# Optimization experiments

Hardware: AMD Instinct MI355X
Metric: run time of the kernel (lower is better)

## Reference

```python
import jax, jax.numpy as jnp
import numpy as np

N_NODES = 1_000_000
FEAT = 128
CONTENT = 256
S2 = 8192          # seed layer (layer 2)
FAN = 8            # sampled neighbors per node (plus self)
S1 = S2 * (FAN + 1)    # 73728
S0 = S1 * (FAN + 1)    # 663552


def _block_edges(key, n_dst, n_src):
    # NodeFlow block: each dst node has a self-edge (its copy sits at the same
    # index in the source layer) plus FAN randomly sampled source neighbors.
    rand_src = jax.random.randint(key, (n_dst * FAN,), 0, n_src, dtype=jnp.int32)
    src = jnp.concatenate([jnp.arange(n_dst, dtype=jnp.int32), rand_src])
    dst = jnp.concatenate([jnp.arange(n_dst, dtype=jnp.int32),
                           jnp.repeat(jnp.arange(n_dst, dtype=jnp.int32), FAN)])
    return src, dst


def setup_inputs() -> dict:
    key = jax.random.key(0)
    ks = jax.random.split(key, 16)
    node_emb = jax.random.normal(ks[0], (N_NODES + 1, FEAT), jnp.float32) / FEAT
    content0 = jax.random.normal(ks[1], (S0, CONTENT), jnp.float32)
    Wp = jax.random.normal(ks[2], (FEAT, CONTENT), jnp.float32) * 0.05
    bp = jnp.zeros((FEAT,), jnp.float32)
    W0 = jax.random.normal(ks[3], (FEAT, 2 * FEAT), jnp.float32) * 0.05
    b0 = jnp.zeros((FEAT,), jnp.float32)
    Wagg0 = jax.random.normal(ks[4], (FEAT, FEAT), jnp.float32) * 0.05
    bagg0 = jnp.zeros((FEAT,), jnp.float32)
    W1 = jax.random.normal(ks[5], (FEAT, 2 * FEAT), jnp.float32) * 0.05
    b1 = jnp.zeros((FEAT,), jnp.float32)
    Wagg1 = jax.random.normal(ks[6], (FEAT, FEAT), jnp.float32) * 0.05
    bagg1 = jnp.zeros((FEAT,), jnp.float32)
    parent0 = jax.random.randint(ks[7], (S0,), 0, N_NODES, dtype=jnp.int32)
    src0, dst0 = _block_edges(ks[8], S1, S0)
    src1, dst1 = _block_edges(ks[9], S2, S1)
    return dict(node_emb=node_emb, content0=content0, Wp=Wp, bp=bp,
                W0=W0, b0=b0, Wagg0=Wagg0, bagg0=bagg0,
                W1=W1, b1=b1, Wagg1=Wagg1, bagg1=bagg1,
                parent0=parent0, src0=src0, dst0=dst0, src1=src1, dst1=dst1)


def _leaky(x):
    return jax.nn.leaky_relu(x, negative_slope=0.1)


def _conv(h_src, h_dst, src, dst, n_dst, W, b, Wagg, bagg, last):
    # message: copy_src('h'), copy_src('one'); reduce: sum -> h_agg, w
    agg = jax.ops.segment_sum(h_src[src], dst, num_segments=n_dst)
    w = jax.ops.segment_sum(jnp.ones((src.shape[0],), h_src.dtype), dst,
                            num_segments=n_dst)[:, None]
    h_agg = (agg - h_dst) / jnp.maximum(w - 1.0, 1.0)
    h_new = jnp.concatenate([h_dst, h_agg], axis=1) @ W.T + b
    h_a = h_agg @ Wagg.T + bagg
    if not last:
        h_new = _leaky(h_new)
        h_a = _leaky(h_a)
    h_new = h_new + h_a
    if last:  # prediction layer: no normalization
        return h_new
    norm = jnp.linalg.norm(h_new, axis=1, keepdims=True)
    return h_new / jnp.clip(norm, 1e-6)


def reference(node_emb, content0, Wp, bp, W0, b0, Wagg0, bagg0,
              W1, b1, Wagg1, bagg1, parent0, src0, dst0, src1, dst1):
    # init h per layer: node embedding + projected content (eval: no dropout/noise)
    h0 = node_emb[parent0 + 1] + _leaky(content0 @ Wp.T + bp)  # [S0, F]
    # layer 1 / 2 nodes are the first S1 / S2 entries of layer 0 (nested parents)
    h1_init = h0[:S1]
    h2_init = h0[:S2]
    h1 = _conv(h0, h1_init, src0, dst0, S1, W0, b0, Wagg0, bagg0, last=False)
    out = _conv(h1, h2_init, src1, dst1, S2, W1, b1, Wagg1, bagg1, last=True)
    return out
```

## Files before the change

kernel.cpp:

```cpp
#include <hip/hip_runtime.h>
#include <hip/hip_bf16.h>
#include <stdint.h>

#define S0N 663552
#define S1N 73728
#define S2N 8192

typedef __attribute__((ext_vector_type(8))) short bf16x8;
typedef __attribute__((ext_vector_type(4))) float floatx4;

static constexpr int LDK = 72;

__device__ __forceinline__ unsigned short f2b(float f) {
    union { float f; unsigned u; } v; v.f = f;
    unsigned r = v.u + 0x7fffu + ((v.u >> 16) & 1u);
    return (unsigned short)(r >> 16);
}
__device__ __forceinline__ float b2f(unsigned short h) {
    union { unsigned u; float f; } v; v.u = ((unsigned)h) << 16;
    return v.f;
}

__device__ __forceinline__ void stage_f32(const float* __restrict__ g, int rowStride,
                                          unsigned short* lds, int tid) {
    int r = tid >> 4;
    const int c = (tid & 15) << 2;
    #pragma unroll
    for (int it = 0; it < 8; ++it, r += 16) {
        const float4 v = *(const float4*)(g + (size_t)r * rowStride + c);
        unsigned short* d = &lds[r * LDK + c];
        d[0] = f2b(v.x); d[1] = f2b(v.y); d[2] = f2b(v.z); d[3] = f2b(v.w);
    }
}

__device__ __forceinline__ void stage_b16(const unsigned short* __restrict__ g, int rowStride,
                                          unsigned short* lds, int tid) {
    int r = tid >> 3;
    const int c = (tid & 7) << 3;
    #pragma unroll
    for (int it = 0; it < 4; ++it, r += 32) {
        const uint4 v = *(const uint4*)(g + (size_t)r * rowStride + c);
        *(uint4*)&lds[r * LDK + c] = v;
    }
}

__device__ __forceinline__ void mfma_128x128(const unsigned short* __restrict__ As,
                                             const unsigned short* __restrict__ Bs,
                                             floatx4 (&acc)[2][8],
                                             int wave, int l15, int quad) {
    #pragma unroll
    for (int kc = 0; kc < 64; kc += 32) {
        bf16x8 a[2], b[8];
        #pragma unroll
        for (int mt = 0; mt < 2; ++mt)
            a[mt] = *(const bf16x8*)&As[(wave * 32 + mt * 16 + l15) * LDK + kc + quad * 8];
        #pragma unroll
        for (int nt = 0; nt < 8; ++nt)
            b[nt] = *(const bf16x8*)&Bs[(nt * 16 + l15) * LDK + kc + quad * 8];
        #pragma unroll
        for (int mt = 0; mt < 2; ++mt)
            #pragma unroll
            for (int nt = 0; nt < 8; ++nt)
                acc[mt][nt] = __builtin_amdgcn_mfma_f32_16x16x32_bf16(a[mt], b[nt], acc[mt][nt], 0, 0, 0);
    }
}

__global__ __launch_bounds__(256, 2) void k_h0(
    const float* __restrict__ content, const float* __restrict__ Wp,
    const float* __restrict__ bp, const float* __restrict__ node_emb,
    const int* __restrict__ parent0, unsigned short* __restrict__ h0)
{
    __shared__ unsigned short As[128 * LDK];
    __shared__ unsigned short Bs[128 * LDK];
    const int tid = threadIdx.x;
    const int wave = tid >> 6, lane = tid & 63;
    const int l15 = lane & 15, quad = lane >> 4;
    const int row0 = blockIdx.x * 128;

    floatx4 acc[2][8];
    #pragma unroll
    for (int i = 0; i < 2; ++i)
        #pragma unroll
        for (int j = 0; j < 8; ++j) acc[i][j] = (floatx4)0.f;

    for (int k0 = 0; k0 < 256; k0 += 64) {
        stage_f32(content + (size_t)row0 * 256 + k0, 256, As, tid);
        stage_f32(Wp + k0, 256, Bs, tid);
        __syncthreads();
        mfma_128x128(As, Bs, acc, wave, l15, quad);
        __syncthreads();
    }

    #pragma unroll
    for (int mt = 0; mt < 2; ++mt) {
        #pragma unroll
        for (int r = 0; r < 4; ++r) {
            const int grow = row0 + wave * 32 + mt * 16 + quad * 4 + r;
            const int p = parent0[grow] + 1;
            const float* ne = node_emb + (size_t)p * 128;
            unsigned short* orow = h0 + (size_t)grow * 128;
            #pragma unroll
            for (int nt = 0; nt < 8; ++nt) {
                const int col = nt * 16 + l15;
                float v = acc[mt][nt][r] + bp[col];
                v = v > 0.f ? v : 0.1f * v;
                v += ne[col];
                orow[col] = f2b(v);
            }
        }
    }
}

__global__ __launch_bounds__(256, 4) void k_gather(
    const unsigned short* __restrict__ hsrc, const int* __restrict__ srcIdx,
    int randOff, const unsigned short* __restrict__ hself,
    const unsigned short* __restrict__ hsub, unsigned short* __restrict__ out)
{
    const int wave = threadIdx.x >> 6, lane = threadIdx.x & 63;
    const int d = blockIdx.x * 4 + wave;
    const int c2 = lane * 2;
    int idx[8];
    #pragma unroll
    for (int j = 0; j < 8; ++j) idx[j] = srcIdx[randOff + d * 8 + j];
    unsigned v[8];
    #pragma unroll
    for (int j = 0; j < 8; ++j)
        v[j] = *(const unsigned*)(hsrc + (size_t)idx[j] * 128 + c2);
    float ax = 0.f, ay = 0.f;
    #pragma unroll
    for (int j = 0; j < 8; ++j) {
        ax += b2f((unsigned short)(v[j] & 0xffffu));
        ay += b2f((unsigned short)(v[j] >> 16));
    }
    if (hself) {
        const unsigned s = *(const unsigned*)(hself + (size_t)d * 128 + c2);
        const unsigned u = *(const unsigned*)(hsub + (size_t)d * 128 + c2);
        ax += b2f((unsigned short)(s & 0xffffu)) - b2f((unsigned short)(u & 0xffffu));
        ay += b2f((unsigned short)(s >> 16))     - b2f((unsigned short)(u >> 16));
    }
    ax *= 0.125f; ay *= 0.125f;
    *(unsigned*)(out + (size_t)d * 128 + c2) =
        (unsigned)f2b(ax) | ((unsigned)f2b(ay) << 16);
}

template<bool LAST>
__global__ __launch_bounds__(256, 2) void k_combine(
    const unsigned short* __restrict__ A1, const unsigned short* __restrict__ A2,
    const float* __restrict__ W, const float* __restrict__ b,
    const float* __restrict__ Wagg, const float* __restrict__ bagg,
    unsigned short* __restrict__ outB, float* __restrict__ outF)
{
    __shared__ unsigned short As[128 * LDK];
    __shared__ unsigned short Bs[128 * LDK];
    __shared__ unsigned short Bs2[128 * LDK];
    const int tid = threadIdx.x;
    const int wave = tid >> 6, lane = tid & 63;
    const int l15 = lane & 15, quad = lane >> 4;
    const int row0 = blockIdx.x * 128;

    floatx4 acc1[2][8], acc2[2][8];
    #pragma unroll
    for (int i = 0; i < 2; ++i)
        #pragma unroll
        for (int j = 0; j < 8; ++j) { acc1[i][j] = (floatx4)0.f; acc2[i][j] = (floatx4)0.f; }

    for (int k0 = 0; k0 < 128; k0 += 64) {
        stage_b16(A1 + (size_t)row0 * 128 + k0, 128, As, tid);
        stage_f32(W + k0, 256, Bs, tid);
        __syncthreads();
        mfma_128x128(As, Bs, acc1, wave, l15, quad);
        __syncthreads();
    }
    for (int k0 = 0; k0 < 128; k0 += 64) {
        stage_b16(A2 + (size_t)row0 * 128 + k0, 128, As, tid);
        stage_f32(W + 128 + k0, 256, Bs, tid);
        stage_f32(Wagg + k0, 128, Bs2, tid);
        __syncthreads();
        mfma_128x128(As, Bs,  acc1, wave, l15, quad);
        mfma_128x128(As, Bs2, acc2, wave, l15, quad);
        __syncthreads();
    }

    #pragma unroll
    for (int mt = 0; mt < 2; ++mt) {
        #pragma unroll
        for (int r = 0; r < 4; ++r) {
            const int grow = row0 + wave * 32 + mt * 16 + quad * 4 + r;
            float h[8]; float ssq = 0.f;
            #pragma unroll
            for (int nt = 0; nt < 8; ++nt) {
                const int col = nt * 16 + l15;
                float v1 = acc1[mt][nt][r] + b[col];
                float v2 = acc2[mt][nt][r] + bagg[col];
                if (!LAST) {
                    v1 = v1 > 0.f ? v1 : 0.1f * v1;
                    v2 = v2 > 0.f ? v2 : 0.1f * v2;
                }
                h[nt] = v1 + v2;
                ssq += h[nt] * h[nt];
            }
            if (LAST) {
                float* orow = outF + (size_t)grow * 128;
                #pragma unroll
                for (int nt = 0; nt < 8; ++nt) orow[nt * 16 + l15] = h[nt];
            } else {
                ssq += __shfl_xor(ssq, 1);
                ssq += __shfl_xor(ssq, 2);
                ssq += __shfl_xor(ssq, 4);
                ssq += __shfl_xor(ssq, 8);
                const float scale = 1.f / fmaxf(sqrtf(ssq), 1e-6f);
                unsigned short* orow = outB + (size_t)grow * 128;
                #pragma unroll
                for (int nt = 0; nt < 8; ++nt) orow[nt * 16 + l15] = f2b(h[nt] * scale);
            }
        }
    }
}

extern "C" void kernel_launch(void* const* d_in, const int* in_sizes, int n_in,
                              void* d_out, int out_size, void* d_ws, size_t ws_size,
                              hipStream_t stream)
{
    const float* node_emb = (const float*)d_in[0];
    const float* content0 = (const float*)d_in[1];
    const float* Wp    = (const float*)d_in[2];
    const float* bp    = (const float*)d_in[3];
    const float* W0    = (const float*)d_in[4];
    const float* b0    = (const float*)d_in[5];
    const float* Wagg0 = (const float*)d_in[6];
    const float* bagg0 = (const float*)d_in[7];
    const float* W1    = (const float*)d_in[8];
    const float* b1    = (const float*)d_in[9];
    const float* Wagg1 = (const float*)d_in[10];
    const float* bagg1 = (const float*)d_in[11];
    const int* parent0 = (const int*)d_in[12];
    const int* src0    = (const int*)d_in[13];
    const int* src1    = (const int*)d_in[15];

    unsigned short* h0    = (unsigned short*)d_ws;
    unsigned short* h1    = h0 + (size_t)S0N * 128;
    unsigned short* hagg0 = h1 + (size_t)S1N * 128;
    unsigned short* hagg1 = hagg0 + (size_t)S1N * 128;

    k_h0<<<S0N / 128, 256, 0, stream>>>(content0, Wp, bp, node_emb, parent0, h0);
    k_gather<<<S1N / 4, 256, 0, stream>>>(h0, src0, S1N, nullptr, nullptr, hagg0);
    k_combine<false><<<S1N / 128, 256, 0, stream>>>(h0, hagg0, W0, b0, Wagg0, bagg0, h1, nullptr);
    k_gather<<<S2N / 4, 256, 0, stream>>>(h1, src1, S2N, h1, h0, hagg1);
    k_combine<true><<<S2N / 128, 256, 0, stream>>>(h0, hagg1, W1, b1, Wagg1, bagg1, nullptr, (float*)d_out);
}
```

Before: 1.346 ms.

## Load A operands directly from global, stage full weights once, coalesce h0 epilogue

Measured after the change: 1.379 ms. 1.02x slower.

```diff
diff --git a/kernel.cpp b/kernel.cpp
--- a/kernel.cpp
+++ b/kernel.cpp
@@ -8,8 +8,6 @@
 
 typedef __attribute__((ext_vector_type(8))) short bf16x8;
 typedef __attribute__((ext_vector_type(4))) float floatx4;
-
-static constexpr int LDK = 72;
 
 __device__ __forceinline__ unsigned short f2b(float f) {
     union { float f; unsigned u; } v; v.f = f;
@@ -20,49 +18,13 @@
     union { unsigned u; float f; } v; v.u = ((unsigned)h) << 16;
     return v.f;
 }
-
-__device__ __forceinline__ void stage_f32(const float* __restrict__ g, int rowStride,
-                                          unsigned short* lds, int tid) {
-    int r = tid >> 4;
-    const int c = (tid & 15) << 2;
-    #pragma unroll
-    for (int it = 0; it < 8; ++it, r += 16) {
-        const float4 v = *(const float4*)(g + (size_t)r * rowStride + c);
-        unsigned short* d = &lds[r * LDK + c];
-        d[0] = f2b(v.x); d[1] = f2b(v.y); d[2] = f2b(v.z); d[3] = f2b(v.w);
-    }
-}
-
-__device__ __forceinline__ void stage_b16(const unsigned short* __restrict__ g, int rowStride,
-                                          unsigned short* lds, int tid) {
-    int r = tid >> 3;
-    const int c = (tid & 7) << 3;
-    #pragma unroll
-    for (int it = 0; it < 4; ++it, r += 32) {
-        const uint4 v = *(const uint4*)(g + (size_t)r * rowStride + c);
-        *(uint4*)&lds[r * LDK + c] = v;
-    }
-}
-
-__device__ __forceinline__ void mfma_128x128(const unsigned short* __restrict__ As,
-                                             const unsigned short* __restrict__ Bs,
-                                             floatx4 (&acc)[2][8],
-                                             int wave, int l15, int quad) {
-    #pragma unroll
-    for (int kc = 0; kc < 64; kc += 32) {
-        bf16x8 a[2], b[8];
-        #pragma unroll
-        for (int mt = 0; mt < 2; ++mt)
-            a[mt] = *(const bf16x8*)&As[(wave * 32 + mt * 16 + l15) * LDK + kc + quad * 8];
-        #pragma unroll
-        for (int nt = 0; nt < 8; ++nt)
-            b[nt] = *(const bf16x8*)&Bs[(nt * 16 + l15) * LDK + kc + quad * 8];
-        #pragma unroll
-        for (int mt = 0; mt < 2; ++mt)
-            #pragma unroll
-            for (int nt = 0; nt < 8; ++nt)
-                acc[mt][nt] = __builtin_amdgcn_mfma_f32_16x16x32_bf16(a[mt], b[nt], acc[mt][nt], 0, 0, 0);
-    }
+__device__ __forceinline__ bf16x8 pack8(float4 a, float4 b) {
+    bf16x8 r;
+    r[0] = (short)f2b(a.x); r[1] = (short)f2b(a.y);
+    r[2] = (short)f2b(a.z); r[3] = (short)f2b(a.w);
+    r[4] = (short)f2b(b.x); r[5] = (short)f2b(b.y);
+    r[6] = (short)f2b(b.z); r[7] = (short)f2b(b.w);
+    return r;
 }
 
 __global__ __launch_bounds__(256, 2) void k_h0(
@@ -70,43 +32,84 @@
     const float* __restrict__ bp, const float* __restrict__ node_emb,
     const int* __restrict__ parent0, unsigned short* __restrict__ h0)
 {
-    __shared__ unsigned short As[128 * LDK];
-    __shared__ unsigned short Bs[128 * LDK];
+    __shared__ unsigned short Bs[128 * 264];
     const int tid = threadIdx.x;
     const int wave = tid >> 6, lane = tid & 63;
     const int l15 = lane & 15, quad = lane >> 4;
     const int row0 = blockIdx.x * 128;
 
+    {
+        const int r = tid >> 1, cb = (tid & 1) * 128;
+        const float* src = Wp + r * 256 + cb;
+        unsigned short* dst = &Bs[r * 264 + cb];
+        #pragma unroll
+        for (int i = 0; i < 32; ++i) {
+            const float4 v = ((const float4*)src)[i];
+            ushort4 o; o.x = f2b(v.x); o.y = f2b(v.y); o.z = f2b(v.z); o.w = f2b(v.w);
+            ((ushort4*)dst)[i] = o;
+        }
+    }
+    __syncthreads();
+
     floatx4 acc[2][8];
     #pragma unroll
     for (int i = 0; i < 2; ++i)
         #pragma unroll
         for (int j = 0; j < 8; ++j) acc[i][j] = (floatx4)0.f;
 
-    for (int k0 = 0; k0 < 256; k0 += 64) {
-        stage_f32(content + (size_t)row0 * 256 + k0, 256, As, tid);
-        stage_f32(Wp + k0, 256, Bs, tid);
-        __syncthreads();
-        mfma_128x128(As, Bs, acc, wave, l15, quad);
-        __syncthreads();
-    }
-
-    #pragma unroll
-    for (int mt = 0; mt < 2; ++mt) {
+    const int arow = row0 + wave * 32;
+    #pragma unroll
+    for (int kc = 0; kc < 8; ++kc) {
+        bf16x8 a[2];
+        #pragma unroll
+        for (int mt = 0; mt < 2; ++mt) {
+            const float* ap = content + (size_t)(arow + mt * 16 + l15) * 256 + kc * 32 + quad * 8;
+            a[mt] = pack8(((const float4*)ap)[0], ((const float4*)ap)[1]);
+        }
+        #pragma unroll
+        for (int nt = 0; nt < 8; ++nt) {
+            const bf16x8 b = *(const bf16x8*)&Bs[(nt * 16 + l15) * 264 + kc * 32 + quad * 8];
+            #pragma unroll
+            for (int mt = 0; mt < 2; ++mt)
+                acc[mt][nt] = __builtin_amdgcn_mfma_f32_16x16x32_bf16(a[mt], b, acc[mt][nt], 0, 0, 0);
+        }
+    }
+
+    __syncthreads();
+    float* T = (float*)Bs;
+    float bpv[8];
+    #pragma unroll
+    for (int nt = 0; nt < 8; ++nt) bpv[nt] = bp[nt * 16 + l15];
+    #pragma unroll
+    for (int mt = 0; mt < 2; ++mt)
         #pragma unroll
         for (int r = 0; r < 4; ++r) {
-            const int grow = row0 + wave * 32 + mt * 16 + quad * 4 + r;
-            const int p = parent0[grow] + 1;
-            const float* ne = node_emb + (size_t)p * 128;
-            unsigned short* orow = h0 + (size_t)grow * 128;
+            const int lrow = wave * 32 + mt * 16 + quad * 4 + r;
             #pragma unroll
             for (int nt = 0; nt < 8; ++nt) {
-                const int col = nt * 16 + l15;
-                float v = acc[mt][nt][r] + bp[col];
+                float v = acc[mt][nt][r] + bpv[nt];
                 v = v > 0.f ? v : 0.1f * v;
-                v += ne[col];
-                orow[col] = f2b(v);
-            }
+                T[lrow * 132 + nt * 16 + l15] = v;
+            }
+        }
+    __syncthreads();
+    {
+        const int r = tid >> 1, cb = (tid & 1) * 64;
+        const int grow = row0 + r;
+        const float* ne = node_emb + (size_t)(parent0[grow] + 1) * 128 + cb;
+        unsigned short* orow = h0 + (size_t)grow * 128 + cb;
+        #pragma unroll
+        for (int i = 0; i < 8; ++i) {
+            const float4 t0 = *(const float4*)&T[r * 132 + cb + i * 8];
+            const float4 t1 = *(const float4*)&T[r * 132 + cb + i * 8 + 4];
+            const float4 n0 = ((const float4*)ne)[2 * i];
+            const float4 n1 = ((const float4*)ne)[2 * i + 1];
+            union { ushort u[8]; uint4 q; } o;
+            o.u[0] = f2b(t0.x + n0.x); o.u[1] = f2b(t0.y + n0.y);
+            o.u[2] = f2b(t0.z + n0.z); o.u[3] = f2b(t0.w + n0.w);
+            o.u[4] = f2b(t1.x + n1.x); o.u[5] = f2b(t1.y + n1.y);
+            o.u[6] = f2b(t1.z + n1.z); o.u[7] = f2b(t1.w + n1.w);
+            *(uint4*)(orow + i * 8) = o.q;
         }
     }
 }
@@ -141,6 +144,19 @@
     ax *= 0.125f; ay *= 0.125f;
     *(unsigned*)(out + (size_t)d * 128 + c2) =
         (unsigned)f2b(ax) | ((unsigned)f2b(ay) << 16);
+}
+
+__device__ __forceinline__ void stageB128(const float* __restrict__ W, int ldw,
+                                          unsigned short* lds, int tid) {
+    const int r = tid >> 1, cb = (tid & 1) * 64;
+    const float* src = W + r * ldw + cb;
+    unsigned short* dst = lds + r * 136 + cb;
+    #pragma unroll
+    for (int i = 0; i < 16; ++i) {
+        const float4 v = ((const float4*)src)[i];
+        ushort4 o; o.x = f2b(v.x); o.y = f2b(v.y); o.z = f2b(v.z); o.w = f2b(v.w);
+        ((ushort4*)dst)[i] = o;
+    }
 }
 
 template<bool LAST>
@@ -150,13 +166,13 @@
     const float* __restrict__ Wagg, const float* __restrict__ bagg,
     unsigned short* __restrict__ outB, float* __restrict__ outF)
 {
-    __shared__ unsigned short As[128 * LDK];
-    __shared__ unsigned short Bs[128 * LDK];
-    __shared__ unsigned short Bs2[128 * LDK];
+    __shared__ unsigned short BsA[128 * 136];
+    __shared__ unsigned short BsB[128 * 136];
     const int tid = threadIdx.x;
     const int wave = tid >> 6, lane = tid & 63;
     const int l15 = lane & 15, quad = lane >> 4;
     const int row0 = blockIdx.x * 128;
+    const int arow = row0 + wave * 32;
 
     floatx4 acc1[2][8], acc2[2][8];
     #pragma unroll
@@ -164,21 +180,43 @@
         #pragma unroll
         for (int j = 0; j < 8; ++j) { acc1[i][j] = (floatx4)0.f; acc2[i][j] = (floatx4)0.f; }
 
-    for (int k0 = 0; k0 < 128; k0 += 64) {
-        stage_b16(A1 + (size_t)row0 * 128 + k0, 128, As, tid);
-        stage_f32(W + k0, 256, Bs, tid);
-        __syncthreads();
-        mfma_128x128(As, Bs, acc1, wave, l15, quad);
-        __syncthreads();
-    }
-    for (int k0 = 0; k0 < 128; k0 += 64) {
-        stage_b16(A2 + (size_t)row0 * 128 + k0, 128, As, tid);
-        stage_f32(W + 128 + k0, 256, Bs, tid);
-        stage_f32(Wagg + k0, 128, Bs2, tid);
-        __syncthreads();
-        mfma_128x128(As, Bs,  acc1, wave, l15, quad);
-        mfma_128x128(As, Bs2, acc2, wave, l15, quad);
-        __syncthreads();
+    stageB128(W, 256, BsA, tid);
+    stageB128(Wagg, 128, BsB, tid);
+    __syncthreads();
+
+    #pragma unroll
+    for (int kc = 0; kc < 4; ++kc) {
+        bf16x8 a[2];
+        #pragma unroll
+        for (int mt = 0; mt < 2; ++mt)
+            a[mt] = *(const bf16x8*)(A1 + (size_t)(arow + mt * 16 + l15) * 128 + kc * 32 + quad * 8);
+        #pragma unroll
+        for (int nt = 0; nt < 8; ++nt) {
+            const bf16x8 bb = *(const bf16x8*)&BsA[(nt * 16 + l15) * 136 + kc * 32 + quad * 8];
+            #pragma unroll
+            for (int mt = 0; mt < 2; ++mt)
+                acc1[mt][nt] = __builtin_amdgcn_mfma_f32_16x16x32_bf16(a[mt], bb, acc1[mt][nt], 0, 0, 0);
+        }
+    }
+    __syncthreads();
+    stageB128(W + 128, 256, BsA, tid);
+    __syncthreads();
+    #pragma unroll
+    for (int kc = 0; kc < 4; ++kc) {
+        bf16x8 a[2];
+        #pragma unroll
+        for (int mt = 0; mt < 2; ++mt)
+            a[mt] = *(const bf16x8*)(A2 + (size_t)(arow + mt * 16 + l15) * 128 + kc * 32 + quad * 8);
+        #pragma unroll
+        for (int nt = 0; nt < 8; ++nt) {
+            const bf16x8 b1v = *(const bf16x8*)&BsA[(nt * 16 + l15) * 136 + kc * 32 + quad * 8];
+            const bf16x8 b2v = *(const bf16x8*)&BsB[(nt * 16 + l15) * 136 + kc * 32 + quad * 8];
+            #pragma unroll
+            for (int mt = 0; mt < 2; ++mt) {
+                acc1[mt][nt] = __builtin_amdgcn_mfma_f32_16x16x32_bf16(a[mt], b1v, acc1[mt][nt], 0, 0, 0);
+                acc2[mt][nt] = __builtin_amdgcn_mfma_f32_16x16x32_bf16(a[mt], b2v, acc2[mt][nt], 0, 0, 0);
+            }
+        }
     }
 
     #pragma unroll
```
